# Performance work log

Measured on AMD Instinct MI355X. Metric: run time of the kernel, lower is better.

The kernel has to match this reference:

```python
import jax, jax.numpy as jnp
import numpy as np

N = 40000      # nodes
E = 640000     # edges (avg degree 16)
D_IN = 256     # input_size
H = 128        # hidden_size
C = 64         # num_classes
L = 2          # num_middle_layers


def spmm(val, row, col, mat):
    # sparse [N,N] @ dense [N,D]: gather neighbor rows, scale, scatter-add
    return jax.ops.segment_sum(val[:, None] * mat[col], row, num_segments=mat.shape[0])


def setup_inputs() -> dict:
    key = jax.random.key(0)
    ks = jax.random.split(key, 12)
    x = jax.random.normal(ks[0], (N, D_IN), dtype=jnp.float32)
    edge_row = jax.random.randint(ks[1], (E,), 0, N)
    edge_col = jax.random.randint(ks[2], (E,), 0, N)
    edge_val = jax.random.uniform(ks[3], (E,), dtype=jnp.float32) / 16.0  # ~normalized adjacency
    # Linear params (stored [in, out]; math equivalent to torch x @ W.T + b)
    w1 = jax.random.normal(ks[4], (D_IN, H), dtype=jnp.float32) * (1.0 / np.sqrt(D_IN))
    b1 = jax.random.normal(ks[5], (H,), dtype=jnp.float32) * 0.01
    wm = jax.random.normal(ks[6], (L, H, H), dtype=jnp.float32) * (1.0 / np.sqrt(H))
    bm = jax.random.normal(ks[7], (L, H), dtype=jnp.float32) * 0.01
    w2 = jax.random.normal(ks[8], (H, C), dtype=jnp.float32) * (1.0 / np.sqrt(H))
    b2 = jax.random.normal(ks[9], (C,), dtype=jnp.float32) * 0.01
    time_step = jnp.array(0.1, dtype=jnp.float32)
    return {"x": x, "edge_row": edge_row, "edge_col": edge_col, "edge_val": edge_val,
            "w1": w1, "b1": b1, "wm": wm, "bm": bm, "w2": w2, "b2": b2,
            "time_step": time_step}


def reference(x, edge_row, edge_col, edge_val, w1, b1, wm, bm, w2, b2, time_step):
    # dropout p=0 -> identity
    h = jax.nn.relu(spmm(edge_val, edge_row, edge_col, x @ w1 + b1))
    for i in range(L):  # residual middle layers: x <- x + relu(A @ (x W + b)) * dt
        f = jax.nn.relu(spmm(edge_val, edge_row, edge_col, h @ wm[i] + bm[i]))
        h = h + f * time_step
    return spmm(edge_val, edge_row, edge_col, h @ w2 + b2)
```

## Files before the change

### kernel.cpp

```cpp
#include <hip/hip_runtime.h>


#define DIN 256
#define HID 128
#define NCLS 64
#define VAL_DEC 1.9073486328125e-6f
#define SB 256

typedef __attribute__((ext_vector_type(8))) short bf16x8;
typedef __attribute__((ext_vector_type(4))) float f32x4;

static __device__ __forceinline__ float bf2f(unsigned int u) {
    return __uint_as_float(u << 16);
}
static __device__ __forceinline__ unsigned short f2bf(float f) {
    unsigned int i = __float_as_uint(f);
    return (unsigned short)((i + 0x7FFFu + ((i >> 16) & 1u)) >> 16);
}
static __device__ __forceinline__ unsigned int pack2(float a, float b) {
    return (unsigned int)f2bf(a) | ((unsigned int)f2bf(b) << 16);
}

__global__ __launch_bounds__(256) void prep_hist_kernel(
        const float* __restrict__ w1, const float* __restrict__ wm,
        const float* __restrict__ w2, unsigned short* __restrict__ w1t,
        unsigned short* __restrict__ wmt, unsigned short* __restrict__ w2t, int L,
        const int* __restrict__ erow, int* __restrict__ counts_t, int E, int NB) {
    __shared__ int cnt[256];
    const int tid = threadIdx.x;
    for (int k = tid; k < NB; k += 256) cnt[k] = 0;

    const int n1 = DIN * HID;
    const int n2 = n1 + L * HID * HID;
    const int n3 = n2 + HID * NCLS;
    for (int idx = blockIdx.x * 256 + tid; idx < n3; idx += SB * 256) {
        if (idx < n1) {
            int n = idx / DIN, k = idx - n * DIN;
            w1t[idx] = f2bf(w1[(size_t)k * HID + n]);
        } else if (idx < n2) {
            int j = idx - n1;
            int i = j / (HID * HID), r = j - i * (HID * HID);
            int n = r / HID, k = r - n * HID;
            wmt[j] = f2bf(wm[(size_t)i * HID * HID + (size_t)k * HID + n]);
        } else {
            int j = idx - n2;
            int n = j / HID, k = j - n * HID;
            w2t[j] = f2bf(w2[(size_t)k * NCLS + n]);
        }
    }
    __syncthreads();
    const int chunk = (E + SB - 1) / SB;
    const int lo = blockIdx.x * chunk;
    const int hi = min(lo + chunk, E);
    for (int e = lo + tid; e < hi; e += 256)
        atomicAdd(&cnt[erow[e] >> 8], 1);
    __syncthreads();
    for (int k = tid; k < NB; k += 256)
        counts_t[k * SB + blockIdx.x] = cnt[k];
}

__global__ __launch_bounds__(1024) void scan_sums_kernel(
        const int* __restrict__ a, int* __restrict__ bsums, int n) {
    __shared__ int wsum[16];
    const int lane = threadIdx.x & 63;
    const int wid  = threadIdx.x >> 6;
    int i = blockIdx.x * 1024 + threadIdx.x;
    int v = (i < n) ? a[i] : 0;
    #pragma unroll
    for (int d = 32; d >= 1; d >>= 1) v += __shfl_xor(v, d, 64);
    if (lane == 0) wsum[wid] = v;
    __syncthreads();
    if (threadIdx.x == 0) {
        int s = 0;
        #pragma unroll
        for (int w = 0; w < 16; ++w) s += wsum[w];
        bsums[blockIdx.x] = s;
    }
}

__global__ __launch_bounds__(1024) void scan_fix_kernel(
        const int* __restrict__ a, const int* __restrict__ bsums,
        int* __restrict__ out, int n, int nb) {
    __shared__ int wsum[16];
    __shared__ int bpref_s;
    const int lane = threadIdx.x & 63;
    const int wid  = threadIdx.x >> 6;
    const int b = blockIdx.x;
    if (wid == 0) {
        int v = (lane < nb && lane < b) ? bsums[lane] : 0;
        #pragma unroll
        for (int d = 32; d >= 1; d >>= 1) v += __shfl_xor(v, d, 64);
        if (lane == 0) bpref_s = v;
    }
    int i = b * 1024 + (int)threadIdx.x;
    int v = (i < n) ? a[i] : 0;
    int incl = v;
    #pragma unroll
    for (int d = 1; d < 64; d <<= 1) {
        int t = __shfl_up(incl, d, 64);
        if (lane >= d) incl += t;
    }
    if (lane == 63) wsum[wid] = incl;
    __syncthreads();
    int wpref = 0;
    #pragma unroll
    for (int w = 0; w < 16; ++w)
        if (w < wid) wpref += wsum[w];
    int excl = bpref_s + wpref + incl - v;
    if (i < n) out[i] = excl;
    if (i == n) out[n] = excl;
}

__global__ __launch_bounds__(256) void mega_kernel(
        const float* __restrict__ x, const unsigned short* __restrict__ w1t,
        const float* __restrict__ b1, unsigned short* __restrict__ z,
        const int* __restrict__ erow, const int* __restrict__ ecol,
        const float* __restrict__ eval, const int* __restrict__ starts,
        unsigned int* __restrict__ bw, unsigned char* __restrict__ br,
        int E, int NB, int gemmBlocks) {
    const int tid = threadIdx.x;
    if ((int)blockIdx.x >= gemmBlocks) {
        __shared__ int ptr[256];
        const int sb = blockIdx.x - gemmBlocks;
        for (int k = tid; k < NB; k += 256) ptr[k] = starts[k * SB + sb];
        __syncthreads();
        const int chunk = (E + SB - 1) / SB;
        const int lo = sb * chunk;
        const int hi = min(lo + chunk, E);
        for (int e = lo + tid; e < hi; e += 256) {
            int r = erow[e];
            int q = min((int)(eval[e] * 524288.0f + 0.5f), 32767);
            unsigned int w = ((unsigned int)ecol[e] << 15) | (unsigned int)q;
            int p = atomicAdd(&ptr[r >> 8], 1);
            bw[p] = w;
            br[p] = (unsigned char)(r & 255);
        }
        return;
    }
    __shared__ __align__(16) unsigned short Alds[64 * 40];
    __shared__ __align__(16) unsigned short Blds[128 * 40];
    const int bm   = blockIdx.x * 64;
    const int wave = tid >> 6;
    const int lane = tid & 63;
    const int m16  = lane & 15;
    const int quad = lane >> 4;
    const int ar = tid >> 2, ac = (tid & 3) * 8;

    f32x4 acc[8] = {};
    for (int k0 = 0; k0 < DIN; k0 += 32) {
        float4 a0 = *(const float4*)&x[(size_t)(bm + ar) * DIN + k0 + ac];
        float4 a1 = *(const float4*)&x[(size_t)(bm + ar) * DIN + k0 + ac + 4];
        uint4 av;
        av.x = pack2(a0.x, a0.y); av.y = pack2(a0.z, a0.w);
        av.z = pack2(a1.x, a1.y); av.w = pack2(a1.z, a1.w);
        *(uint4*)&Alds[ar * 40 + ac] = av;
        #pragma unroll
        for (int i = 0; i < 2; ++i) {
            int c = tid + 256 * i;
            int brow = c >> 2, bc = (c & 3) * 8;
            *(uint4*)&Blds[brow * 40 + bc] = *(const uint4*)&w1t[(size_t)brow * DIN + k0 + bc];
        }
        __syncthreads();
        bf16x8 af = *(const bf16x8*)&Alds[(wave * 16 + m16) * 40 + quad * 8];
        #pragma unroll
        for (int j = 0; j < 8; ++j) {
            bf16x8 bfr = *(const bf16x8*)&Blds[(j * 16 + m16) * 40 + quad * 8];
            acc[j] = __builtin_amdgcn_mfma_f32_16x16x32_bf16(af, bfr, acc[j], 0, 0, 0);
        }
        __syncthreads();
    }
    #pragma unroll
    for (int j = 0; j < 8; ++j) {
        int col = j * 16 + m16;
        float bb = b1[col];
        #pragma unroll
        for (int r = 0; r < 4; ++r) {
            int row = bm + wave * 16 + quad * 4 + r;
            z[(size_t)row * HID + col] = f2bf(acc[j][r] + bb);
        }
    }
}

__global__ __launch_bounds__(256) void finalize_kernel(
        const int* __restrict__ starts, const unsigned int* __restrict__ bw,
        const unsigned char* __restrict__ br, unsigned int* __restrict__ edges,
        int* __restrict__ offs, int N, int NB) {
    __shared__ int cnt[256];
    __shared__ int posl[256];
    __shared__ int ws[4];
    const int tid = threadIdx.x;
    const int k = blockIdx.x;
    const int b0 = starts[k * SB];
    const int b1 = starts[(k + 1) * SB];
    cnt[tid] = 0;
    __syncthreads();
    for (int i = b0 + tid; i < b1; i += 256)
        atomicAdd(&cnt[br[i]], 1);
    __syncthreads();
    const int lane = tid & 63, wid = tid >> 6;
    int v = cnt[tid];
    int incl = v;
    #pragma unroll
    for (int d = 1; d < 64; d <<= 1) {
        int t = __shfl_up(incl, d, 64);
        if (lane >= d) incl += t;
    }
    if (lane == 63) ws[wid] = incl;
    __syncthreads();
    int wp = 0;
    #pragma unroll
    for (int w = 0; w < 4; ++w)
        if (w < wid) wp += ws[w];
    int excl = wp + incl - v;
    int g = (k << 8) + tid;
    if (g <= N) offs[g] = b0 + excl;
    posl[tid] = b0 + excl;
    __syncthreads();
    for (int i = b0 + tid; i < b1; i += 256) {
        int r = br[i];
        unsigned int w = bw[i];
        int p = atomicAdd(&posl[r], 1);
        edges[p] = w;
    }
}

template <int BN>
__global__ __launch_bounds__(256) void gemm_mfma_kernel(
        const unsigned short* __restrict__ A, const unsigned short* __restrict__ Wt,
        const float* __restrict__ bias, unsigned short* __restrict__ C, int K) {
    constexpr int NT = BN / 16;
    __shared__ __align__(16) unsigned short Alds[64 * 40];
    __shared__ __align__(16) unsigned short Blds[BN * 40];
    const int tid  = threadIdx.x;
    const int bm   = blockIdx.x * 64;
    const int wave = tid >> 6;
    const int lane = tid & 63;
    const int m16  = lane & 15;
    const int quad = lane >> 4;
    const int ar = tid >> 2, ac = (tid & 3) * 8;

    f32x4 acc[NT] = {};
    for (int k0 = 0; k0 < K; k0 += 32) {
        uint4 av = *(const uint4*)&A[(size_t)(bm + ar) * K + k0 + ac];
        *(uint4*)&Alds[ar * 40 + ac] = av;
        #pragma unroll
        for (int i = 0; i < BN / 64; ++i) {
            int c = tid + 256 * i;
            int brow = c >> 2, bc = (c & 3) * 8;
            *(uint4*)&Blds[brow * 40 + bc] = *(const uint4*)&Wt[(size_t)brow * K + k0 + bc];
        }
        __syncthreads();
        bf16x8 af = *(const bf16x8*)&Alds[(wave * 16 + m16) * 40 + quad * 8];
        #pragma unroll
        for (int j = 0; j < NT; ++j) {
            bf16x8 bfr = *(const bf16x8*)&Blds[(j * 16 + m16) * 40 + quad * 8];
            acc[j] = __builtin_amdgcn_mfma_f32_16x16x32_bf16(af, bfr, acc[j], 0, 0, 0);
        }
        __syncthreads();
    }
    #pragma unroll
    for (int j = 0; j < NT; ++j) {
        int col = j * 16 + m16;
        float bb = bias[col];
        #pragma unroll
        for (int r = 0; r < 4; ++r) {
            int row = bm + wave * 16 + quad * 4 + r;
            C[(size_t)row * BN + col] = f2bf(acc[j][r] + bb);
        }
    }
}

template <int D, int MODE>
__global__ __launch_bounds__(256) void spmm_kernel(
        const int* __restrict__ offs, const unsigned int* __restrict__ edges,
        const unsigned short* __restrict__ z,
        float* __restrict__ out, unsigned short* __restrict__ hb,
        const float* __restrict__ dt_ptr, int n) {
    int r = (int)((blockIdx.x * blockDim.x + threadIdx.x) >> 6);
    int lane = threadIdx.x & 63;
    if (r >= n) return;
    r = __builtin_amdgcn_readfirstlane(r);
    const int s = offs[r], e = offs[r + 1];
    float acc0 = 0.f, acc1 = 0.f;
    int p = s;
    if (D == 128) {
        const unsigned int* z32 = (const unsigned int*)z;
        for (; p + 8 <= e; p += 8) {
            unsigned int ev[8], g[8];
            #pragma unroll
            for (int i = 0; i < 8; ++i) ev[i] = __builtin_nontemporal_load(edges + p + i);
            #pragma unroll
            for (int i = 0; i < 8; ++i)
                g[i] = z32[(size_t)(ev[i] >> 15) * 64 + lane];
            #pragma unroll
            for (int i = 0; i < 8; ++i) {
                float v = (float)(ev[i] & 0x7fffu) * VAL_DEC;
                acc0 = fmaf(v, bf2f(g[i] & 0xffffu), acc0);
                acc1 = fmaf(v, bf2f(g[i] >> 16), acc1);
            }
        }
        for (; p < e; ++p) {
            unsigned int ev = __builtin_nontemporal_load(edges + p);
            float v = (float)(ev & 0x7fffu) * VAL_DEC;
            unsigned int g = z32[(size_t)(ev >> 15) * 64 + lane];
            acc0 = fmaf(v, bf2f(g & 0xffffu), acc0);
            acc1 = fmaf(v, bf2f(g >> 16), acc1);
        }
        unsigned int* hbw = (unsigned int*)hb + (size_t)r * 64 + lane;
        if (MODE == 2) {
            float2 o; o.x = acc0; o.y = acc1;
            *(float2*)&out[(size_t)r * 128 + 2 * lane] = o;
        } else if (MODE == 0) {
            *hbw = pack2(fmaxf(acc0, 0.f), fmaxf(acc1, 0.f));
        } else {
            float dt = *dt_ptr;
            unsigned int cur = *hbw;
            float f0 = bf2f(cur & 0xffffu) + fmaxf(acc0, 0.f) * dt;
            float f1 = bf2f(cur >> 16)    + fmaxf(acc1, 0.f) * dt;
            *hbw = pack2(f0, f1);
        }
    } else {
        for (; p + 8 <= e; p += 8) {
            unsigned int ev[8];
            unsigned short g[8];
            #pragma unroll
            for (int i = 0; i < 8; ++i) ev[i] = __builtin_nontemporal_load(edges + p + i);
            #pragma unroll
            for (int i = 0; i < 8; ++i)
                g[i] = z[(size_t)(ev[i] >> 15) * 64 + lane];
            #pragma unroll
            for (int i = 0; i < 8; ++i)
                acc0 = fmaf((float)(ev[i] & 0x7fffu) * VAL_DEC, bf2f(g[i]), acc0);
        }
        for (; p < e; ++p) {
            unsigned int ev = __builtin_nontemporal_load(edges + p);
            acc0 = fmaf((float)(ev & 0x7fffu) * VAL_DEC,
                        bf2f((unsigned int)z[(size_t)(ev >> 15) * 64 + lane]), acc0);
        }
        out[(size_t)r * 64 + lane] = acc0;
    }
}

extern "C" void kernel_launch(void* const* d_in, const int* in_sizes, int n_in,
                              void* d_out, int out_size, void* d_ws, size_t ws_size,
                              hipStream_t stream) {
    const float* x    = (const float*)d_in[0];
    const int*   erow = (const int*)d_in[1];
    const int*   ecol = (const int*)d_in[2];
    const float* eval = (const float*)d_in[3];
    const float* w1   = (const float*)d_in[4];
    const float* b1   = (const float*)d_in[5];
    const float* wm   = (const float*)d_in[6];
    const float* bmp  = (const float*)d_in[7];
    const float* w2   = (const float*)d_in[8];
    const float* b2   = (const float*)d_in[9];
    const float* dt   = (const float*)d_in[10];

    const int N = in_sizes[0] / DIN;
    const int E = in_sizes[1];
    const int L = in_sizes[7] / HID;
    const int NB = (N + 255) >> 8;

    float* outp = (float*)d_out;

    char* ws = (char*)d_ws;
    auto carve = [&](size_t bytes) -> char* {
        char* p = ws;
        ws += (bytes + 255) & ~(size_t)255;
        return p;
    };
    int*            counts = (int*)carve((size_t)(NB * SB + 1) * 4);
    int*            starts = (int*)carve((size_t)(NB * SB + 1) * 4);
    int*            bsums  = (int*)carve(64 * 4);
    int*            offs   = (int*)carve((size_t)(N + 1) * 4);
    unsigned int*   bw     = (unsigned int*)carve((size_t)E * 4);
    unsigned char*  brr    = (unsigned char*)carve((size_t)E);
    unsigned int*   edges  = (unsigned int*)carve((size_t)E * 4);
    unsigned short* z      = (unsigned short*)carve((size_t)N * HID * 2);
    unsigned short* hb     = (unsigned short*)carve((size_t)N * HID * 2);
    unsigned short* w1t    = (unsigned short*)carve((size_t)HID * DIN * 2);
    unsigned short* wmt    = (unsigned short*)carve((size_t)L * HID * HID * 2);
    unsigned short* w2t    = (unsigned short*)carve((size_t)NCLS * HID * 2);

    const int nscan   = NB * SB;
    const int ntiles  = (nscan + 1023) / 1024;
    const int gemm_blocks = N / 64;
    const int spmm_blocks = (N + 3) / 4;

    prep_hist_kernel<<<SB, 256, 0, stream>>>(w1, wm, w2, w1t, wmt, w2t, L,
                                             erow, counts, E, NB);
    scan_sums_kernel<<<ntiles, 1024, 0, stream>>>(counts, bsums, nscan);
    scan_fix_kernel<<<ntiles, 1024, 0, stream>>>(counts, bsums, starts, nscan, ntiles);
    mega_kernel<<<gemm_blocks + SB, 256, 0, stream>>>(
        x, w1t, b1, z, erow, ecol, eval, starts, bw, brr, E, NB, gemm_blocks);
    finalize_kernel<<<NB, 256, 0, stream>>>(starts, bw, brr, edges, offs, N, NB);

    spmm_kernel<HID, 0><<<spmm_blocks, 256, 0, stream>>>(offs, edges, z, nullptr, hb, nullptr, N);

    for (int i = 0; i < L; ++i) {
        gemm_mfma_kernel<HID><<<gemm_blocks, 256, 0, stream>>>(
            hb, wmt + (size_t)i * HID * HID, bmp + (size_t)i * HID, z, HID);
        spmm_kernel<HID, 1><<<spmm_blocks, 256, 0, stream>>>(offs, edges, z, nullptr, hb, dt, N);
    }

    gemm_mfma_kernel<NCLS><<<gemm_blocks, 256, 0, stream>>>(hb, w2t, b2, z, HID);
    spmm_kernel<NCLS, 2><<<spmm_blocks, 256, 0, stream>>>(offs, edges, z, outp, nullptr, nullptr, N);
}
```

Before: 264.9 us.

## Keep full weight tile resident in LDS and read A directly from global

The MFMA GEMM now loads the whole K=128 weight matrix into LDS once per block and loops over row tiles with a grid-stride loop. A fragments are read straight from global memory instead of being staged through LDS. This removes the per-K-step barriers and repeated weight reloads. In exchange the larger LDS footprint may lower occupancy, and with the unchanged launch of N/64 blocks each block still handles only one tile, so the weight load is not amortised.

```diff
diff --git a/kernel.cpp b/kernel.cpp
--- a/kernel.cpp
+++ b/kernel.cpp
@@ -227,45 +227,45 @@
 template <int BN>
 __global__ __launch_bounds__(256) void gemm_mfma_kernel(
         const unsigned short* __restrict__ A, const unsigned short* __restrict__ Wt,
-        const float* __restrict__ bias, unsigned short* __restrict__ C, int K) {
+        const float* __restrict__ bias, unsigned short* __restrict__ C, int N) {
     constexpr int NT = BN / 16;
-    __shared__ __align__(16) unsigned short Alds[64 * 40];
-    __shared__ __align__(16) unsigned short Blds[BN * 40];
+    constexpr int K = 128;
+    __shared__ __align__(16) unsigned short Blds[BN * 136];
     const int tid  = threadIdx.x;
-    const int bm   = blockIdx.x * 64;
     const int wave = tid >> 6;
     const int lane = tid & 63;
     const int m16  = lane & 15;
     const int quad = lane >> 4;
-    const int ar = tid >> 2, ac = (tid & 3) * 8;
-
-    f32x4 acc[NT] = {};
-    for (int k0 = 0; k0 < K; k0 += 32) {
-        uint4 av = *(const uint4*)&A[(size_t)(bm + ar) * K + k0 + ac];
-        *(uint4*)&Alds[ar * 40 + ac] = av;
-        #pragma unroll
-        for (int i = 0; i < BN / 64; ++i) {
-            int c = tid + 256 * i;
-            int brow = c >> 2, bc = (c & 3) * 8;
-            *(uint4*)&Blds[brow * 40 + bc] = *(const uint4*)&Wt[(size_t)brow * K + k0 + bc];
-        }
-        __syncthreads();
-        bf16x8 af = *(const bf16x8*)&Alds[(wave * 16 + m16) * 40 + quad * 8];
+
+    for (int c = tid; c < BN * 16; c += 256) {
+        int brow = c >> 4, bc = (c & 15) * 8;
+        *(uint4*)&Blds[brow * 136 + bc] = *(const uint4*)&Wt[(size_t)brow * K + bc];
+    }
+    __syncthreads();
+
+    const int tiles = N >> 6;
+    for (int t = blockIdx.x; t < tiles; t += gridDim.x) {
+        const int arow = t * 64 + wave * 16 + m16;
+        const unsigned short* ap = A + (size_t)arow * K + quad * 8;
+        f32x4 acc[NT] = {};
+        #pragma unroll
+        for (int s = 0; s < 4; ++s) {
+            bf16x8 af = *(const bf16x8*)(ap + s * 32);
+            #pragma unroll
+            for (int j = 0; j < NT; ++j) {
+                bf16x8 bfr = *(const bf16x8*)&Blds[(j * 16 + m16) * 136 + s * 32 + quad * 8];
+                acc[j] = __builtin_amdgcn_mfma_f32_16x16x32_bf16(af, bfr, acc[j], 0, 0, 0);
+            }
+        }
         #pragma unroll
         for (int j = 0; j < NT; ++j) {
-            bf16x8 bfr = *(const bf16x8*)&Blds[(j * 16 + m16) * 40 + quad * 8];
-            acc[j] = __builtin_amdgcn_mfma_f32_16x16x32_bf16(af, bfr, acc[j], 0, 0, 0);
-        }
-        __syncthreads();
-    }
-    #pragma unroll
-    for (int j = 0; j < NT; ++j) {
-        int col = j * 16 + m16;
-        float bb = bias[col];
-        #pragma unroll
-        for (int r = 0; r < 4; ++r) {
-            int row = bm + wave * 16 + quad * 4 + r;
-            C[(size_t)row * BN + col] = f2bf(acc[j][r] + bb);
+            int col = j * 16 + m16;
+            float bb = bias[col];
+            #pragma unroll
+            for (int r = 0; r < 4; ++r) {
+                int row = t * 64 + wave * 16 + quad * 4 + r;
+                C[(size_t)row * BN + col] = f2bf(acc[j][r] + bb);
+            }
         }
     }
 }
@@ -399,10 +399,10 @@
 
     for (int i = 0; i < L; ++i) {
         gemm_mfma_kernel<HID><<<gemm_blocks, 256, 0, stream>>>(
-            hb, wmt + (size_t)i * HID * HID, bmp + (size_t)i * HID, z, HID);
+            hb, wmt + (size_t)i * HID * HID, bmp + (size_t)i * HID, z, N);
         spmm_kernel<HID, 1><<<spmm_blocks, 256, 0, stream>>>(offs, edges, z, nullptr, hb, dt, N);
     }
 
-    gemm_mfma_kernel<NCLS><<<gemm_blocks, 256, 0, stream>>>(hb, w2t, b2, z, HID);
+    gemm_mfma_kernel<NCLS><<<gemm_blocks, 256, 0, stream>>>(hb, w2t, b2, z, N);
     spmm_kernel<NCLS, 2><<<spmm_blocks, 256, 0, stream>>>(offs, edges, z, outp, nullptr, nullptr, N);
 }
```

New measurement: 275.0 us. 1.04x slower.
